# Kernel optimization log

Measured on AMD Instinct MI355X. Metric: run time of the kernel, lower is better.

## Reference

```python
import jax, jax.numpy as jnp
import numpy as np

H = 16  # num_heads

def _toroidal_bias(S, dtype):
    # float mask: +1.0 at (i, (i-1)%S), (i,i), (i, (i+1)%S); PyTorch ADDS float attn_mask to scores
    eye = jnp.eye(S, dtype=dtype)
    return eye + jnp.roll(eye, 1, axis=1) + jnp.roll(eye, -1, axis=1)

def setup_inputs() -> dict:
    key = jax.random.key(0)
    ks = jax.random.split(key, 7)
    E = 1024
    S, B = 2048, 2
    sc = 0.02
    return {
        "x": jax.random.normal(ks[0], (S, B, E), dtype=jnp.float32),
        "w_tor": jax.random.normal(ks[1], (E, E), dtype=jnp.float32) * sc,
        "b_tor": jax.random.normal(ks[2], (E,), dtype=jnp.float32) * sc,
        "in_proj_w": jax.random.normal(ks[3], (3 * E, E), dtype=jnp.float32) * sc,
        "in_proj_b": jax.random.normal(ks[4], (3 * E,), dtype=jnp.float32) * sc,
        "out_w": jax.random.normal(ks[5], (E, E), dtype=jnp.float32) * sc,
        "out_b": jax.random.normal(ks[6], (E,), dtype=jnp.float32) * sc,
    }

def reference(x, w_tor, b_tor, in_proj_w, in_proj_b, out_w, out_b):
    S, B, E = x.shape
    hd = E // H
    scale = 1.0 / jnp.sqrt(jnp.asarray(hd, dtype=x.dtype))
    # toroidal projection, then fused in_proj (self-attention: q=k=v=x_toroidal)
    xt = x @ w_tor.T + b_tor                      # (S,B,E)
    qkv = xt @ in_proj_w.T + in_proj_b            # (S,B,3E)
    q, k, v = jnp.split(qkv, 3, axis=-1)
    def to_heads(t):
        return t.reshape(S, B, H, hd).transpose(1, 2, 0, 3)  # (B,H,S,hd)
    q, k, v = to_heads(q), to_heads(k), to_heads(v)
    bias = _toroidal_bias(S, x.dtype)             # (S,S) additive float mask
    scores = jnp.einsum('bhqd,bhkd->bhqk', q * scale, k) + bias
    attn = jax.nn.softmax(scores, axis=-1)
    o = jnp.einsum('bhqk,bhkd->bhqd', attn, v)    # (B,H,S,hd)
    o = o.transpose(2, 0, 1, 3).reshape(S, B, E)
    return o @ out_w.T + out_b
```

## Files before the change

kernel.cpp:

```cpp
#include <hip/hip_runtime.h>

#define S_LEN 2048
#define NB    2
#define EMB   1024
#define NH    16
#define HD    64

typedef __bf16 bf16_t;
typedef bf16_t bf16x8 __attribute__((ext_vector_type(8)));
typedef bf16_t bf16x4v __attribute__((ext_vector_type(4)));
typedef float  f32x4  __attribute__((ext_vector_type(4)));
typedef float  f32x16 __attribute__((ext_vector_type(16)));

#define L2E 1.44269504f

__device__ __forceinline__ void g2l16(const void* g, void* l) {
    auto gp = reinterpret_cast<const unsigned int __attribute__((address_space(1)))*>(
        reinterpret_cast<uintptr_t>(g));
    auto lp = reinterpret_cast<unsigned int __attribute__((address_space(3)))*>(
        reinterpret_cast<uintptr_t>(l));
    __builtin_amdgcn_global_load_lds(gp, lp, 16, 0, 0);
}

__global__ __launch_bounds__(256) void cast4_f32_bf16(
    const float* __restrict__ s0, bf16_t* __restrict__ d0,
    const float* __restrict__ s1, bf16_t* __restrict__ d1,
    const float* __restrict__ s2, bf16_t* __restrict__ d2,
    const float* __restrict__ s3, bf16_t* __restrict__ d3)
{
    long i = (long)blockIdx.x * 256 + threadIdx.x;
    const float* s; bf16_t* d; long off;
    if (i < 1048576)      { s = s0; d = d0; off = i; }
    else if (i < 1310720) { s = s1; d = d1; off = i - 1048576; }
    else if (i < 2097152) { s = s2; d = d2; off = i - 1310720; }
    else                  { s = s3; d = d3; off = i - 2097152; }
    float4 v = ((const float4*)s)[off];
    bf16x4v o;
    o[0] = (bf16_t)v.x; o[1] = (bf16_t)v.y; o[2] = (bf16_t)v.z; o[3] = (bf16_t)v.w;
    *(bf16x4v*)(d + off * 4) = o;
}

template<int TN, int MODE>
__global__ __launch_bounds__(256) void gemm_bt_bf16(
    const bf16_t* __restrict__ A, const bf16_t* __restrict__ W,
    const float* __restrict__ bias, void* __restrict__ Cout,
    bf16_t* __restrict__ Qp, bf16_t* __restrict__ Kp, bf16_t* __restrict__ Vtp,
    int M, int N, int K)
{
    constexpr int MB = (TN == 128) ? 4 : 2;
    __shared__ __align__(16) bf16_t As[2][128 * 32];
    __shared__ __align__(16) bf16_t Bs[2][TN * 32];

    const int tid  = threadIdx.x;
    const int lane = tid & 63;
    const int w    = tid >> 6;
    const int lm   = lane & 15;
    const int lq   = lane >> 4;
    const long m0  = (long)blockIdx.y * 128;
    const long n0  = (long)blockIdx.x * TN;
    const int wm0  = (TN == 128) ? (w >> 1) * 64 : w * 32;
    const int wn0  = (TN == 128) ? (w & 1) * 64 : 0;

    f32x4 acc[MB][4];
#pragma unroll
    for (int i = 0; i < MB; ++i)
#pragma unroll
        for (int j = 0; j < 4; ++j) acc[i][j] = (f32x4){0.f, 0.f, 0.f, 0.f};

    auto stage = [&](int k0, int buf) {
        bf16_t* asb = &As[buf][0];
        bf16_t* bsb = &Bs[buf][0];
#pragma unroll
        for (int j = 0; j < 2; ++j) {
            int a   = (w * 2 + j) * 64 + lane;
            int row = a >> 2;
            int c   = (a & 3) ^ ((row >> 1) & 3);
            g2l16(A + (m0 + row) * K + k0 + c * 8, asb + (w * 2 + j) * 512);
        }
#pragma unroll
        for (int j = 0; j < TN / 64; ++j) {
            int a   = (w * (TN / 64) + j) * 64 + lane;
            int row = a >> 2;
            int c   = (a & 3) ^ ((row >> 1) & 3);
            g2l16(W + (n0 + row) * K + k0 + c * 8, bsb + (w * (TN / 64) + j) * 512);
        }
    };

    stage(0, 0);
    for (int k0 = 0; k0 < K; k0 += 32) {
        const int cur = (k0 >> 5) & 1;
        asm volatile("s_waitcnt vmcnt(0)" ::: "memory");
        __syncthreads();
        if (k0 + 32 < K) stage(k0 + 32, cur ^ 1);

        bf16x8 af[MB], bfr[4];
#pragma unroll
        for (int mb = 0; mb < MB; ++mb) {
            int r = wm0 + mb * 16 + lm;
            af[mb] = *(const bf16x8*)&As[cur][r * 32 + ((lq ^ ((r >> 1) & 3)) << 3)];
        }
#pragma unroll
        for (int nb = 0; nb < 4; ++nb) {
            int r = wn0 + nb * 16 + lm;
            bfr[nb] = *(const bf16x8*)&Bs[cur][r * 32 + ((lq ^ ((r >> 1) & 3)) << 3)];
        }
#pragma unroll
        for (int mb = 0; mb < MB; ++mb)
#pragma unroll
            for (int nb = 0; nb < 4; ++nb)
                acc[mb][nb] = __builtin_amdgcn_mfma_f32_16x16x32_bf16(
                    af[mb], bfr[nb], acc[mb][nb], 0, 0, 0);
    }

    float b4[4];
#pragma unroll
    for (int nb = 0; nb < 4; ++nb) b4[nb] = bias[n0 + wn0 + nb * 16 + lm];

#pragma unroll
    for (int mb = 0; mb < MB; ++mb) {
#pragma unroll
        for (int r = 0; r < 4; ++r) {
            long m = m0 + wm0 + mb * 16 + lq * 4 + r;
#pragma unroll
            for (int nb = 0; nb < 4; ++nb) {
                int n   = (int)n0 + wn0 + nb * 16 + lm;
                float v = acc[mb][nb][r] + b4[nb];
                if (MODE == 0) {
                    ((float*)Cout)[m * N + n] = v;
                } else if (MODE == 1) {
                    ((bf16_t*)Cout)[m * N + n] = (bf16_t)v;
                } else {
                    int sec  = n >> 10;
                    int nloc = n & 1023;
                    int h    = nloc >> 6;
                    int d    = nloc & 63;
                    int s    = (int)(m >> 1), b = (int)(m & 1);
                    int bh   = b * 16 + h;
                    if (sec == 0) {
                        Qp[((size_t)(bh * S_LEN + s)) * 64 + d] =
                            (bf16_t)(v * (0.125f * L2E));
                    } else if (sec == 1) {
                        Kp[((size_t)(bh * S_LEN + s)) * 64 + d] = (bf16_t)v;
                    } else {
                        Vtp[((size_t)(bh * 64 + d)) * S_LEN + s] = (bf16_t)v;
                    }
                }
            }
        }
    }
}

__global__ __launch_bounds__(256, 2) void attn_mfma(
    const bf16_t* __restrict__ Qb, const bf16_t* __restrict__ Kb,
    const bf16_t* __restrict__ Vtb, bf16_t* __restrict__ O)
{
    __shared__ __align__(16) bf16_t Ks[2][8 * 512];
    __shared__ __align__(16) bf16_t Vts[2][8 * 512];
    __shared__ __align__(16) bf16_t Ps[4][8 * 256];

    const int tid  = threadIdx.x;
    const int lane = tid & 63;
    const int w    = tid >> 6;
    const int bid  = blockIdx.x;
    const int bh   = ((bid & 7) << 2) | (bid >> 7);
    const int qt   = (bid >> 3) & 15;
    const int l5   = lane & 31;
    const int hi   = lane >> 5;

    const int rsub = lane >> 3;
    const int csw  = (lane & 7) ^ rsub;
    int cc[4];
#pragma unroll
    for (int i = 0; i < 4; ++i) cc[i] = ((2 * i + hi) ^ (l5 & 7)) * 8;

    const bf16_t* qrow = Qb + ((size_t)bh * S_LEN + qt * 128 + w * 32 + l5) * 64 + hi * 8;
    bf16x8 qf[4];
#pragma unroll
    for (int ds = 0; ds < 4; ++ds) qf[ds] = *(const bf16x8*)(qrow + ds * 16);

    f32x16 oacc[2];
#pragma unroll
    for (int dh = 0; dh < 2; ++dh)
#pragma unroll
        for (int i = 0; i < 16; ++i) oacc[dh][i] = 0.f;
    float plsum = 0.f;

    auto stageKV = [&](int kt, int buf) {
        bf16_t* ksb = &Ks[buf][0];
        bf16_t* vsb = &Vts[buf][0];
        const bf16_t* kg = Kb + ((size_t)bh * S_LEN + kt * 64) * 64;
        const bf16_t* vg = Vtb + (size_t)bh * 64 * S_LEN + kt * 64;
#pragma unroll
        for (int j = 0; j < 2; ++j) {
            int i = w * 2 + j;
            g2l16(kg + (size_t)(i * 8 + rsub) * 64 + csw * 8,    ksb + i * 512);
            g2l16(vg + (size_t)(i * 8 + rsub) * S_LEN + csw * 8, vsb + i * 512);
        }
    };

    stageKV(0, 0);
    for (int kt = 0; kt < 32; ++kt) {
        const int cur = kt & 1;
        asm volatile("s_waitcnt vmcnt(0)" ::: "memory");
        __syncthreads();
        if (kt < 31) stageKV(kt + 1, cur ^ 1);

        f32x16 sacc[2];
        __builtin_amdgcn_s_setprio(1);
#pragma unroll
        for (int kh = 0; kh < 2; ++kh) {
#pragma unroll
            for (int i = 0; i < 16; ++i) sacc[kh][i] = 0.f;
#pragma unroll
            for (int ds = 0; ds < 4; ++ds) {
                bf16x8 kf = *(const bf16x8*)&Ks[cur][(kh * 32 + l5) * 64 + cc[ds]];
                sacc[kh] = __builtin_amdgcn_mfma_f32_32x32x16_bf16(kf, qf[ds], sacc[kh], 0, 0, 0);
            }
        }
        __builtin_amdgcn_s_setprio(0);

        int ktd = (kt - 2 * qt) & 31;
        if (ktd <= 2 || ktd == 31) {
            int q = qt * 128 + w * 32 + l5;
#pragma unroll
            for (int kh = 0; kh < 2; ++kh)
#pragma unroll
                for (int r = 0; r < 16; ++r) {
                    int key  = kt * 64 + kh * 32 + (r & 3) + 8 * (r >> 2) + 4 * hi;
                    int diff = (key - q) & (S_LEN - 1);
                    if (diff <= 1 || diff == S_LEN - 1) sacc[kh][r] += L2E;
                }
        }

#pragma unroll
        for (int kh = 0; kh < 2; ++kh)
#pragma unroll
            for (int g = 0; g < 4; ++g) {
                bf16x4v pk;
#pragma unroll
                for (int e = 0; e < 4; ++e) {
                    float p = __builtin_amdgcn_exp2f(sacc[kh][g * 4 + e]);
                    plsum += p;
                    pk[e] = (bf16_t)p;
                }
                *(bf16x4v*)&Ps[w][(kh * 4 + g) * 256 + hi * 128 + l5 * 4] = pk;
            }

        bf16x8 pf[4];
#pragma unroll
        for (int ks = 0; ks < 4; ++ks) {
            bf16x4v lo = *(const bf16x4v*)&Ps[w][(2 * ks + hi) * 256 + l5 * 4];
            bf16x4v hb = *(const bf16x4v*)&Ps[w][(2 * ks + hi) * 256 + 128 + l5 * 4];
#pragma unroll
            for (int e = 0; e < 4; ++e) { pf[ks][e] = lo[e]; pf[ks][4 + e] = hb[e]; }
        }
        __builtin_amdgcn_s_setprio(1);
#pragma unroll
        for (int dh = 0; dh < 2; ++dh) {
#pragma unroll
            for (int ks = 0; ks < 4; ++ks) {
                bf16x8 vf = *(const bf16x8*)&Vts[cur][(dh * 32 + l5) * 64 + cc[ks]];
                oacc[dh] = __builtin_amdgcn_mfma_f32_32x32x16_bf16(pf[ks], vf, oacc[dh], 0, 0, 0);
            }
        }
        __builtin_amdgcn_s_setprio(0);
    }

    plsum += __shfl_xor(plsum, 32, 64);
    float* Lw = (float*)&Ps[w][0];
    if (hi == 0) Lw[l5] = plsum;

    float inv16[16];
#pragma unroll
    for (int g = 0; g < 4; ++g) {
        f32x4 lv = *(const f32x4*)&Lw[8 * g + 4 * hi];
#pragma unroll
        for (int e = 0; e < 4; ++e) inv16[g * 4 + e] = 1.0f / lv[e];
    }

    const int b = bh >> 4, h = bh & 15;
#pragma unroll
    for (int dh = 0; dh < 2; ++dh)
#pragma unroll
        for (int r = 0; r < 16; ++r) {
            int qrel = (r & 3) + 8 * (r >> 2) + 4 * hi;
            int s = qt * 128 + w * 32 + qrel;
            O[((size_t)(s * NB + b)) * EMB + h * 64 + dh * 32 + l5] =
                (bf16_t)(oacc[dh][r] * inv16[r]);
        }
}

extern "C" void kernel_launch(void* const* d_in, const int* in_sizes, int n_in,
                              void* d_out, int out_size, void* d_ws, size_t ws_size,
                              hipStream_t stream)
{
    const float* x         = (const float*)d_in[0];
    const float* w_tor     = (const float*)d_in[1];
    const float* b_tor     = (const float*)d_in[2];
    const float* in_proj_w = (const float*)d_in[3];
    const float* in_proj_b = (const float*)d_in[4];
    const float* out_w     = (const float*)d_in[5];
    const float* out_b     = (const float*)d_in[6];
    float* out = (float*)d_out;

    const int M = S_LEN * NB;

    char* base = (char*)d_ws;
    bf16_t* xb    = (bf16_t*)(base);
    bf16_t* wtorb = (bf16_t*)(base + ( 8ull << 20));
    bf16_t* ipwb  = (bf16_t*)(base + (10ull << 20));
    bf16_t* outwb = (bf16_t*)(base + (16ull << 20));
    bf16_t* xtb   = (bf16_t*)(base + (18ull << 20));
    bf16_t* Kb    = (bf16_t*)(base + (26ull << 20));
    bf16_t* Vtb   = (bf16_t*)(base + (34ull << 20));
    bf16_t* Qb    = xb;
    bf16_t* Ob    = xtb;

    cast4_f32_bf16<<<dim3(9216), 256, 0, stream>>>(
        x, xb, w_tor, wtorb, in_proj_w, ipwb, out_w, outwb);

    gemm_bt_bf16<64, 1><<<dim3(EMB / 64, M / 128), 256, 0, stream>>>(
        xb, wtorb, b_tor, xtb, nullptr, nullptr, nullptr, M, EMB, EMB);

    gemm_bt_bf16<128, 2><<<dim3(3 * EMB / 128, M / 128), 256, 0, stream>>>(
        xtb, ipwb, in_proj_b, nullptr, Qb, Kb, Vtb, M, 3 * EMB, EMB);

    attn_mfma<<<dim3(32 * 16), 256, 0, stream>>>(Qb, Kb, Vtb, Ob);

    gemm_bt_bf16<64, 0><<<dim3(EMB / 64, M / 128), 256, 0, stream>>>(
        Ob, outwb, out_b, out, nullptr, nullptr, nullptr, M, EMB, EMB);
}
```

Baseline: 212.1 us.

## Process two 32-query subtiles per wave to reuse K/V fragments in attention

Each wave of the attention kernel now handles 64 query rows as two 32-row subtiles, so every K and V fragment read from LDS feeds two MFMAs. The block covers 256 queries, the grid is halved to 256 blocks, and launch bounds drop to one block per CU to allow more registers. This cuts LDS reads and global K/V staging per query. In exchange, each CU holds fewer resident waves, and the doubled accumulator state raises register pressure, which can weaken latency hiding.

```diff
diff --git a/kernel.cpp b/kernel.cpp
--- a/kernel.cpp
+++ b/kernel.cpp
@@ -150,7 +150,7 @@
     }
 }
 
-__global__ __launch_bounds__(256, 2) void attn_mfma(
+__global__ __launch_bounds__(256, 1) void attn_mfma(
     const bf16_t* __restrict__ Qb, const bf16_t* __restrict__ Kb,
     const bf16_t* __restrict__ Vtb, bf16_t* __restrict__ O)
 {
@@ -162,8 +162,8 @@
     const int lane = tid & 63;
     const int w    = tid >> 6;
     const int bid  = blockIdx.x;
-    const int bh   = ((bid & 7) << 2) | (bid >> 7);
-    const int qt   = (bid >> 3) & 15;
+    const int bh   = ((bid & 7) << 2) | ((bid >> 3) & 3);
+    const int qt   = bid >> 5;
     const int l5   = lane & 31;
     const int hi   = lane >> 5;
 
@@ -173,17 +173,25 @@
 #pragma unroll
     for (int i = 0; i < 4; ++i) cc[i] = ((2 * i + hi) ^ (l5 & 7)) * 8;
 
-    const bf16_t* qrow = Qb + ((size_t)bh * S_LEN + qt * 128 + w * 32 + l5) * 64 + hi * 8;
-    bf16x8 qf[4];
-#pragma unroll
-    for (int ds = 0; ds < 4; ++ds) qf[ds] = *(const bf16x8*)(qrow + ds * 16);
-
-    f32x16 oacc[2];
-#pragma unroll
-    for (int dh = 0; dh < 2; ++dh)
-#pragma unroll
-        for (int i = 0; i < 16; ++i) oacc[dh][i] = 0.f;
-    float plsum = 0.f;
+    const int qbase = qt * 256 + w * 64;
+
+    bf16x8 qf[2][4];
+#pragma unroll
+    for (int qs = 0; qs < 2; ++qs) {
+        const bf16_t* qrow =
+            Qb + ((size_t)bh * S_LEN + qbase + qs * 32 + l5) * 64 + hi * 8;
+#pragma unroll
+        for (int ds = 0; ds < 4; ++ds) qf[qs][ds] = *(const bf16x8*)(qrow + ds * 16);
+    }
+
+    f32x16 oacc[2][2];
+#pragma unroll
+    for (int qs = 0; qs < 2; ++qs)
+#pragma unroll
+        for (int dh = 0; dh < 2; ++dh)
+#pragma unroll
+            for (int i = 0; i < 16; ++i) oacc[qs][dh][i] = 0.f;
+    float plsum[2] = {0.f, 0.f};
 
     auto stageKV = [&](int kt, int buf) {
         bf16_t* ksb = &Ks[buf][0];
@@ -205,89 +213,107 @@
         __syncthreads();
         if (kt < 31) stageKV(kt + 1, cur ^ 1);
 
-        f32x16 sacc[2];
+        f32x16 sacc[2][2];
+#pragma unroll
+        for (int qs = 0; qs < 2; ++qs)
+#pragma unroll
+            for (int kh = 0; kh < 2; ++kh)
+#pragma unroll
+                for (int i = 0; i < 16; ++i) sacc[qs][kh][i] = 0.f;
         __builtin_amdgcn_s_setprio(1);
 #pragma unroll
         for (int kh = 0; kh < 2; ++kh) {
-#pragma unroll
-            for (int i = 0; i < 16; ++i) sacc[kh][i] = 0.f;
 #pragma unroll
             for (int ds = 0; ds < 4; ++ds) {
                 bf16x8 kf = *(const bf16x8*)&Ks[cur][(kh * 32 + l5) * 64 + cc[ds]];
-                sacc[kh] = __builtin_amdgcn_mfma_f32_32x32x16_bf16(kf, qf[ds], sacc[kh], 0, 0, 0);
+                sacc[0][kh] = __builtin_amdgcn_mfma_f32_32x32x16_bf16(kf, qf[0][ds], sacc[0][kh], 0, 0, 0);
+                sacc[1][kh] = __builtin_amdgcn_mfma_f32_32x32x16_bf16(kf, qf[1][ds], sacc[1][kh], 0, 0, 0);
             }
         }
         __builtin_amdgcn_s_setprio(0);
 
-        int ktd = (kt - 2 * qt) & 31;
-        if (ktd <= 2 || ktd == 31) {
-            int q = qt * 128 + w * 32 + l5;
+#pragma unroll
+        for (int qs = 0; qs < 2; ++qs) {
+            int d0 = (kt * 64 - (qbase + qs * 32)) & (S_LEN - 1);
+            if (d0 <= 32 || d0 >= S_LEN - 64) {
+                int q = qbase + qs * 32 + l5;
+#pragma unroll
+                for (int kh = 0; kh < 2; ++kh)
+#pragma unroll
+                    for (int r = 0; r < 16; ++r) {
+                        int key  = kt * 64 + kh * 32 + (r & 3) + 8 * (r >> 2) + 4 * hi;
+                        int diff = (key - q) & (S_LEN - 1);
+                        if (diff <= 1 || diff == S_LEN - 1) sacc[qs][kh][r] += L2E;
+                    }
+            }
+        }
+
+        bf16x8 pf[2][4];
+#pragma unroll
+        for (int qs = 0; qs < 2; ++qs) {
 #pragma unroll
             for (int kh = 0; kh < 2; ++kh)
 #pragma unroll
-                for (int r = 0; r < 16; ++r) {
-                    int key  = kt * 64 + kh * 32 + (r & 3) + 8 * (r >> 2) + 4 * hi;
-                    int diff = (key - q) & (S_LEN - 1);
-                    if (diff <= 1 || diff == S_LEN - 1) sacc[kh][r] += L2E;
+                for (int g = 0; g < 4; ++g) {
+                    float p0 = __builtin_amdgcn_exp2f(sacc[qs][kh][g * 4 + 0]);
+                    float p1 = __builtin_amdgcn_exp2f(sacc[qs][kh][g * 4 + 1]);
+                    float p2 = __builtin_amdgcn_exp2f(sacc[qs][kh][g * 4 + 2]);
+                    float p3 = __builtin_amdgcn_exp2f(sacc[qs][kh][g * 4 + 3]);
+                    plsum[qs] += (p0 + p1) + (p2 + p3);
+                    bf16x4v pk;
+                    pk[0] = (bf16_t)p0; pk[1] = (bf16_t)p1;
+                    pk[2] = (bf16_t)p2; pk[3] = (bf16_t)p3;
+                    *(bf16x4v*)&Ps[w][(kh * 4 + g) * 256 + hi * 128 + l5 * 4] = pk;
                 }
-        }
-
-#pragma unroll
-        for (int kh = 0; kh < 2; ++kh)
-#pragma unroll
-            for (int g = 0; g < 4; ++g) {
-                bf16x4v pk;
-#pragma unroll
-                for (int e = 0; e < 4; ++e) {
-                    float p = __builtin_amdgcn_exp2f(sacc[kh][g * 4 + e]);
-                    plsum += p;
-                    pk[e] = (bf16_t)p;
-                }
-                *(bf16x4v*)&Ps[w][(kh * 4 + g) * 256 + hi * 128 + l5 * 4] = pk;
-            }
-
-        bf16x8 pf[4];
-#pragma unroll
-        for (int ks = 0; ks < 4; ++ks) {
-            bf16x4v lo = *(const bf16x4v*)&Ps[w][(2 * ks + hi) * 256 + l5 * 4];
-            bf16x4v hb = *(const bf16x4v*)&Ps[w][(2 * ks + hi) * 256 + 128 + l5 * 4];
-#pragma unroll
-            for (int e = 0; e < 4; ++e) { pf[ks][e] = lo[e]; pf[ks][4 + e] = hb[e]; }
-        }
+#pragma unroll
+            for (int ks = 0; ks < 4; ++ks) {
+                bf16x4v lo = *(const bf16x4v*)&Ps[w][(2 * ks + hi) * 256 + l5 * 4];
+                bf16x4v hb = *(const bf16x4v*)&Ps[w][(2 * ks + hi) * 256 + 128 + l5 * 4];
+#pragma unroll
+                for (int e = 0; e < 4; ++e) { pf[qs][ks][e] = lo[e]; pf[qs][ks][4 + e] = hb[e]; }
+            }
+        }
+
         __builtin_amdgcn_s_setprio(1);
 #pragma unroll
         for (int dh = 0; dh < 2; ++dh) {
 #pragma unroll
             for (int ks = 0; ks < 4; ++ks) {
                 bf16x8 vf = *(const bf16x8*)&Vts[cur][(dh * 32 + l5) * 64 + cc[ks]];
-                oacc[dh] = __builtin_amdgcn_mfma_f32_32x32x16_bf16(pf[ks], vf, oacc[dh], 0, 0, 0);
+                oacc[0][dh] = __builtin_amdgcn_mfma_f32_32x32x16_bf16(pf[0][ks], vf, oacc[0][dh], 0, 0, 0);
+                oacc[1][dh] = __builtin_amdgcn_mfma_f32_32x32x16_bf16(pf[1][ks], vf, oacc[1][dh], 0, 0, 0);
             }
         }
         __builtin_amdgcn_s_setprio(0);
     }
 
-    plsum += __shfl_xor(plsum, 32, 64);
     float* Lw = (float*)&Ps[w][0];
-    if (hi == 0) Lw[l5] = plsum;
-
-    float inv16[16];
-#pragma unroll
-    for (int g = 0; g < 4; ++g) {
-        f32x4 lv = *(const f32x4*)&Lw[8 * g + 4 * hi];
-#pragma unroll
-        for (int e = 0; e < 4; ++e) inv16[g * 4 + e] = 1.0f / lv[e];
+#pragma unroll
+    for (int qs = 0; qs < 2; ++qs) {
+        float pl = plsum[qs] + __shfl_xor(plsum[qs], 32, 64);
+        if (hi == 0) Lw[qs * 32 + l5] = pl;
     }
 
     const int b = bh >> 4, h = bh & 15;
 #pragma unroll
-    for (int dh = 0; dh < 2; ++dh)
-#pragma unroll
-        for (int r = 0; r < 16; ++r) {
-            int qrel = (r & 3) + 8 * (r >> 2) + 4 * hi;
-            int s = qt * 128 + w * 32 + qrel;
-            O[((size_t)(s * NB + b)) * EMB + h * 64 + dh * 32 + l5] =
-                (bf16_t)(oacc[dh][r] * inv16[r]);
-        }
+    for (int qs = 0; qs < 2; ++qs) {
+        float inv16[16];
+#pragma unroll
+        for (int g = 0; g < 4; ++g) {
+            f32x4 lv = *(const f32x4*)&Lw[qs * 32 + 8 * g + 4 * hi];
+#pragma unroll
+            for (int e = 0; e < 4; ++e) inv16[g * 4 + e] = 1.0f / lv[e];
+        }
+#pragma unroll
+        for (int dh = 0; dh < 2; ++dh)
+#pragma unroll
+            for (int r = 0; r < 16; ++r) {
+                int qrel = (r & 3) + 8 * (r >> 2) + 4 * hi;
+                int s = qbase + qs * 32 + qrel;
+                O[((size_t)(s * NB + b)) * EMB + h * 64 + dh * 32 + l5] =
+                    (bf16_t)(oacc[qs][dh][r] * inv16[r]);
+            }
+    }
 }
 
 extern "C" void kernel_launch(void* const* d_in, const int* in_sizes, int n_in,
@@ -325,7 +351,7 @@
     gemm_bt_bf16<128, 2><<<dim3(3 * EMB / 128, M / 128), 256, 0, stream>>>(
         xtb, ipwb, in_proj_b, nullptr, Qb, Kb, Vtb, M, 3 * EMB, EMB);
 
-    attn_mfma<<<dim3(32 * 16), 256, 0, stream>>>(Qb, Kb, Vtb, Ob);
+    attn_mfma<<<dim3(256), 256, 0, stream>>>(Qb, Kb, Vtb, Ob);
 
     gemm_bt_bf16<64, 0><<<dim3(EMB / 64, M / 128), 256, 0, stream>>>(
         Ob, outwb, out_b, out, nullptr, nullptr, nullptr, M, EMB, EMB);
```

Result: slower. 255.6 us (+20.5%).
